# Performance work log

Measured on AMD Instinct MI355X. Metric: run time of the kernel, lower is better.

The kernel has to match this reference:

```python
import jax, jax.numpy as jnp
import numpy as np

WIN = 9  # local window size per spatial dim

def _boxfilter3d(x):
    k = jnp.ones((1, 1, WIN, WIN, WIN), x.dtype) / float(WIN ** 3)
    return jax.lax.conv_general_dilated(
        x, k, window_strides=(1, 1, 1), padding='SAME',
        dimension_numbers=('NCDHW', 'OIDHW', 'NCDHW'))

def setup_inputs() -> dict:
    key = jax.random.key(0)
    k1, k2 = jax.random.split(key)
    shape = (2, 1, 160, 192, 160)
    y_true = jax.random.uniform(k1, shape, dtype=jnp.float32)
    y_pred = jax.random.uniform(k2, shape, dtype=jnp.float32)
    return {"y_true": y_true, "y_pred": y_pred}

def reference(y_true, y_pred):
    Ii, Ji = y_true, y_pred
    mu1 = _boxfilter3d(Ii)
    mu2 = _boxfilter3d(Ji)
    sigma1_sq = _boxfilter3d(Ii * Ii) - mu1 * mu1
    sigma2_sq = _boxfilter3d(Ji * Ji) - mu2 * mu2
    sigma12 = _boxfilter3d(Ii * Ji) - mu1 * mu2
    cc = (sigma12 * sigma12) / (sigma1_sq * sigma2_sq + 1e-5)
    return -jnp.mean(cc)
```

## Files before the change

### kernel.cpp

```cpp
#include <hip/hip_runtime.h>

#define DD 160
#define HH 192
#define WW 160
#define HWs (HH * WW)
#define NTOT 9830400.0f
#define DOUT 10
#define NIT  18
#define NBLK 1920

#define SDRS 62
#define SDP  1492
#define HSRS 10
#define HSC  162
#define HSP  810

typedef float    v4 __attribute__((ext_vector_type(4)));
typedef _Float16 h4 __attribute__((ext_vector_type(4)));
typedef _Float16 h2 __attribute__((ext_vector_type(2)));
typedef _Float16 h8 __attribute__((ext_vector_type(8)));

__device__ __forceinline__ void block_sync_lds() {
    __builtin_amdgcn_s_waitcnt(0xc07f);
    __builtin_amdgcn_s_barrier();
}
__device__ __forceinline__ v4 up(h4 x) { return __builtin_convertvector(x, v4); }
__device__ __forceinline__ h4 dnp(v4 x) {
    h2 a = __builtin_bit_cast(h2, __builtin_amdgcn_cvt_pkrtz(x[0], x[1]));
    h2 b = __builtin_bit_cast(h2, __builtin_amdgcn_cvt_pkrtz(x[2], x[3]));
    return __builtin_shufflevector(a, b, 0, 1, 2, 3);
}

__global__ __launch_bounds__(256, 4) void kf(const float* __restrict__ I,
                                             const float* __restrict__ J,
                                             float* __restrict__ partial) {
    __shared__ __align__(16) h4 SDL[2 * SDP];
    __shared__ __align__(16) h4 HSL[2 * HSP];
    __shared__ float red[256];

    const int tid = threadIdx.x;
    const int bx = blockIdx.x, by = blockIdx.y, b = blockIdx.z;
    const int w0 = (bx % 5) * 32, h0 = (bx / 5) * 16;
    const int d0 = by * DOUT;
    const int bid = bx + 60 * (by + 16 * b);

    const int rt = tid ^ ((bx & 1) << 7);

    const bool p1 = rt < 240;
    const int r = rt / 10, g = rt % 10;
    const int gh = h0 - 4 + r, gw = w0 - 4 + g * 4;
    const bool colOK = p1 && gh >= 0 && gh < HH && gw >= 0 && gw < WW;
    const size_t colOff = (size_t)gh * WW + gw;
    const float* Ib = I + (size_t)b * DD * HWs + colOff;
    const float* Jb = J + (size_t)b * DD * HWs + colOff;
    const int sdwOff = r * SDRS + (r >> 3) * 2 + 6 * g;

    const bool p2 = rt < 100;
    const int g2 = rt % 10, ch2 = (rt / 10) % 5, hh0 = (rt / 50) * 8;
    const int sdrOff = hh0 * SDRS + (hh0 >> 3) * 2 + 6 * g2 +
                       (ch2 == 4 ? 4 + (g2 & 1) : ch2);
    const int hswOff = ch2 * HSC + hh0 * HSRS + g2;

    const bool p3 = rt >= 128;
    const int q3 = rt & 127;
    const int hh = q3 >> 3, sg = q3 & 7;
    const int hsrOff = hh * HSRS + sg;

    v4 sd0 = 0.f, sd1 = 0.f, sd2 = 0.f, sd3 = 0.f, sd4 = 0.f;
    h4 fI[9], fJ[9];
#pragma unroll
    for (int uu = 0; uu < 9; ++uu) { fI[uu] = (h4)(_Float16)0; fJ[uu] = (h4)(_Float16)0; }
    v4 pLI = 0.f, pLJ = 0.f;
    float acc = 0.f;
    const float inv = 1.0f / 729.0f;

    {
        const int si = d0 - 4;
        if (colOK && si >= 0) {
            pLI = *(const v4*)(Ib + (size_t)si * HWs);
            pLJ = *(const v4*)(Jb + (size_t)si * HWs);
        }
    }

    for (int tb = 0; tb < 27; tb += 9) {
#pragma unroll
        for (int u = 0; u < 9; ++u) {
            const int t = tb + u;
            if (t < NIT + 2) {
                if (t < NIT && p1) {
                    h4 cI = dnp(pLI), cJ = dnp(pLJ);
                    v4 aI = up(cI), aJ = up(cJ);
                    v4 dI = aI, dJv = aJ;
                    v4 dII = aI * aI, dJJ = aJ * aJ, dIJ = aI * aJ;
                    if (t >= 9) {
                        v4 bI = up(fI[u]), bJ = up(fJ[u]);
                        dI -= bI; dJv -= bJ;
                        dII -= bI * bI; dJJ -= bJ * bJ; dIJ -= bI * bJ;
                    }
                    fI[u] = cI; fJ[u] = cJ;
                    sd0 += dI; sd1 += dJv; sd2 += dII; sd3 += dJJ; sd4 += dIJ;
                    h4* const qb = &SDL[(t & 1) * SDP + sdwOff];
                    h4 c0 = dnp(sd0), c1 = dnp(sd1), c2 = dnp(sd2), c3 = dnp(sd3);
                    *(h8*)qb       = __builtin_shufflevector(c0, c1, 0,1,2,3,4,5,6,7);
                    *(h8*)(qb + 2) = __builtin_shufflevector(c2, c3, 0,1,2,3,4,5,6,7);
                    qb[4 + (g & 1)] = dnp(sd4);
                    pLI = 0.f; pLJ = 0.f;
                    const int sn = d0 - 3 + t;
                    if (t + 1 < NIT && colOK && sn >= 0 && sn < DD) {
                        pLI = *(const v4*)(Ib + (size_t)sn * HWs);
                        pLJ = *(const v4*)(Jb + (size_t)sn * HWs);
                    }
                }

                if (t >= 1 && t <= NIT && p2) {
                    const int par = (t - 1) & 1;
                    const h4* const sdr = &SDL[par * SDP + sdrOff];
                    h4* const hsw = &HSL[par * HSP + hswOff];
                    h4 s = sdr[0];
#pragma unroll
                    for (int k = 1; k < 9; ++k)
                        s += sdr[k * SDRS + (k >= 8 ? 2 : 0)];
                    hsw[0] = s;
#pragma unroll
                    for (int j = 1; j < 8; ++j) {
                        s += sdr[(j + 8) * SDRS + 2]
                           - sdr[(j - 1) * SDRS + (j - 1 >= 8 ? 2 : 0)];
                        hsw[j * HSRS] = s;
                    }
                }

                if (t >= 10 && p3) {
                    const h4* const hsr = &HSL[(t & 1) * HSP + hsrOff];
                    float w[5][4];
#pragma unroll
                    for (int c = 0; c < 5; ++c) {
                        v4 fa = up(hsr[c * HSC]);
                        v4 fb = up(hsr[c * HSC + 1]);
                        v4 fc = up(hsr[c * HSC + 2]);
                        float s = fa[0] + fa[1] + fa[2] + fa[3] +
                                  fb[0] + fb[1] + fb[2] + fb[3] + fc[0];
                        w[c][0] = s;
                        s += fc[1] - fa[0]; w[c][1] = s;
                        s += fc[2] - fa[1]; w[c][2] = s;
                        s += fc[3] - fa[2]; w[c][3] = s;
                    }
#pragma unroll
                    for (int e = 0; e < 4; ++e) {
                        float mu1 = w[0][e] * inv, mu2 = w[1][e] * inv;
                        float g1  = fmaf(-mu1, mu1, w[2][e] * inv);
                        float g2v = fmaf(-mu2, mu2, w[3][e] * inv);
                        float g12 = fmaf(-mu1, mu2, w[4][e] * inv);
                        acc += __fdividef(g12 * g12, fmaf(g1, g2v, 1e-5f));
                    }
                }

                block_sync_lds();
            }
        }
    }

    red[tid] = acc;
    __syncthreads();
    if (tid < 128) red[tid] += red[tid + 128];
    __syncthreads();
    if (tid < 64) {
        float a = red[tid] + red[tid + 64];
#pragma unroll
        for (int off = 32; off > 0; off >>= 1) a += __shfl_down(a, off);
        if (tid == 0) partial[bid] = a;
    }
}

__global__ void k3_final(const float* __restrict__ partial,
                         float* __restrict__ out) {
    __shared__ float r[1024];
    const int i = threadIdx.x;
    float v = (i < NBLK) ? partial[i] : 0.f;
    if (i + 1024 < NBLK) v += partial[i + 1024];
    r[i] = v;
    __syncthreads();
    for (int off = 512; off > 0; off >>= 1) {
        if (i < off) r[i] += r[i + off];
        __syncthreads();
    }
    if (i == 0) out[0] = -r[0] * (1.0f / NTOT);
}

extern "C" void kernel_launch(void* const* d_in, const int* in_sizes, int n_in,
                              void* d_out, int out_size, void* d_ws, size_t ws_size,
                              hipStream_t stream) {
    (void)in_sizes; (void)n_in; (void)out_size; (void)ws_size;
    const float* I = (const float*)d_in[0];
    const float* J = (const float*)d_in[1];
    float* out     = (float*)d_out;
    float* partial = (float*)d_ws;

    dim3 grid(60, 16, 2);
    kf<<<grid, 256, 0, stream>>>(I, J, partial);
    k3_final<<<1, 1024, 0, stream>>>(partial, out);
}
```

Measured before the change: 167.8 us.

## Reload outgoing depth slices from memory, store H-sums in fp32, remap blocks

Drops the register ring of fp16 input values for the sliding depth window and instead reloads the outgoing slice from global memory (likely served from cache). Input values are now used in fp32 without fp16 rounding. The horizontal partial sums go to LDS as fp32 rather than fp16, which doubles that buffer. Blocks move to a 1D grid with an XCD-aware interleaved tile mapping, and launch bounds drop to 3 waves per SIMD. The aim is to cut register pressure and improve L2 locality, at the cost of extra global loads and more LDS use.

```diff
diff --git a/kernel.cpp b/kernel.cpp
--- a/kernel.cpp
+++ b/kernel.cpp
@@ -31,18 +31,20 @@
     return __builtin_shufflevector(a, b, 0, 1, 2, 3);
 }
 
-__global__ __launch_bounds__(256, 4) void kf(const float* __restrict__ I,
+__global__ __launch_bounds__(256, 3) void kf(const float* __restrict__ I,
                                              const float* __restrict__ J,
                                              float* __restrict__ partial) {
     __shared__ __align__(16) h4 SDL[2 * SDP];
-    __shared__ __align__(16) h4 HSL[2 * HSP];
+    __shared__ __align__(16) v4 HSL[2 * HSP];
     __shared__ float red[256];
 
     const int tid = threadIdx.x;
-    const int bx = blockIdx.x, by = blockIdx.y, b = blockIdx.z;
+    const int wgid = blockIdx.x;
+    const int tl = (wgid & 7) * 240 + (wgid >> 3);
+    const int bx = tl % 60, by = (tl / 60) % 16, b = tl / 960;
     const int w0 = (bx % 5) * 32, h0 = (bx / 5) * 16;
     const int d0 = by * DOUT;
-    const int bid = bx + 60 * (by + 16 * b);
+    const int bid = tl;
 
     const int rt = tid ^ ((bx & 1) << 7);
 
@@ -67,10 +69,8 @@
     const int hsrOff = hh * HSRS + sg;
 
     v4 sd0 = 0.f, sd1 = 0.f, sd2 = 0.f, sd3 = 0.f, sd4 = 0.f;
-    h4 fI[9], fJ[9];
-#pragma unroll
-    for (int uu = 0; uu < 9; ++uu) { fI[uu] = (h4)(_Float16)0; fJ[uu] = (h4)(_Float16)0; }
     v4 pLI = 0.f, pLJ = 0.f;
+    v4 pOI = 0.f, pOJ = 0.f;
     float acc = 0.f;
     const float inv = 1.0f / 729.0f;
 
@@ -82,81 +82,78 @@
         }
     }
 
-    for (int tb = 0; tb < 27; tb += 9) {
 #pragma unroll
-        for (int u = 0; u < 9; ++u) {
-            const int t = tb + u;
-            if (t < NIT + 2) {
-                if (t < NIT && p1) {
-                    h4 cI = dnp(pLI), cJ = dnp(pLJ);
-                    v4 aI = up(cI), aJ = up(cJ);
-                    v4 dI = aI, dJv = aJ;
-                    v4 dII = aI * aI, dJJ = aJ * aJ, dIJ = aI * aJ;
-                    if (t >= 9) {
-                        v4 bI = up(fI[u]), bJ = up(fJ[u]);
-                        dI -= bI; dJv -= bJ;
-                        dII -= bI * bI; dJJ -= bJ * bJ; dIJ -= bI * bJ;
-                    }
-                    fI[u] = cI; fJ[u] = cJ;
-                    sd0 += dI; sd1 += dJv; sd2 += dII; sd3 += dJJ; sd4 += dIJ;
-                    h4* const qb = &SDL[(t & 1) * SDP + sdwOff];
-                    h4 c0 = dnp(sd0), c1 = dnp(sd1), c2 = dnp(sd2), c3 = dnp(sd3);
-                    *(h8*)qb       = __builtin_shufflevector(c0, c1, 0,1,2,3,4,5,6,7);
-                    *(h8*)(qb + 2) = __builtin_shufflevector(c2, c3, 0,1,2,3,4,5,6,7);
-                    qb[4 + (g & 1)] = dnp(sd4);
-                    pLI = 0.f; pLJ = 0.f;
-                    const int sn = d0 - 3 + t;
-                    if (t + 1 < NIT && colOK && sn >= 0 && sn < DD) {
-                        pLI = *(const v4*)(Ib + (size_t)sn * HWs);
-                        pLJ = *(const v4*)(Jb + (size_t)sn * HWs);
-                    }
-                }
-
-                if (t >= 1 && t <= NIT && p2) {
-                    const int par = (t - 1) & 1;
-                    const h4* const sdr = &SDL[par * SDP + sdrOff];
-                    h4* const hsw = &HSL[par * HSP + hswOff];
-                    h4 s = sdr[0];
-#pragma unroll
-                    for (int k = 1; k < 9; ++k)
-                        s += sdr[k * SDRS + (k >= 8 ? 2 : 0)];
-                    hsw[0] = s;
-#pragma unroll
-                    for (int j = 1; j < 8; ++j) {
-                        s += sdr[(j + 8) * SDRS + 2]
-                           - sdr[(j - 1) * SDRS + (j - 1 >= 8 ? 2 : 0)];
-                        hsw[j * HSRS] = s;
-                    }
-                }
-
-                if (t >= 10 && p3) {
-                    const h4* const hsr = &HSL[(t & 1) * HSP + hsrOff];
-                    float w[5][4];
-#pragma unroll
-                    for (int c = 0; c < 5; ++c) {
-                        v4 fa = up(hsr[c * HSC]);
-                        v4 fb = up(hsr[c * HSC + 1]);
-                        v4 fc = up(hsr[c * HSC + 2]);
-                        float s = fa[0] + fa[1] + fa[2] + fa[3] +
-                                  fb[0] + fb[1] + fb[2] + fb[3] + fc[0];
-                        w[c][0] = s;
-                        s += fc[1] - fa[0]; w[c][1] = s;
-                        s += fc[2] - fa[1]; w[c][2] = s;
-                        s += fc[3] - fa[2]; w[c][3] = s;
-                    }
-#pragma unroll
-                    for (int e = 0; e < 4; ++e) {
-                        float mu1 = w[0][e] * inv, mu2 = w[1][e] * inv;
-                        float g1  = fmaf(-mu1, mu1, w[2][e] * inv);
-                        float g2v = fmaf(-mu2, mu2, w[3][e] * inv);
-                        float g12 = fmaf(-mu1, mu2, w[4][e] * inv);
-                        acc += __fdividef(g12 * g12, fmaf(g1, g2v, 1e-5f));
-                    }
-                }
-
-                block_sync_lds();
+    for (int t = 0; t < NIT + 2; ++t) {
+        if (t < NIT && p1) {
+            const v4 cI = pLI, cJ = pLJ;
+            v4 dI = cI, dJv = cJ;
+            v4 dII = cI * cI, dJJ = cJ * cJ, dIJ = cI * cJ;
+            if (t >= 9) {
+                dI  -= pOI;        dJv -= pOJ;
+                dII -= pOI * pOI;  dJJ -= pOJ * pOJ;  dIJ -= pOI * pOJ;
+            }
+            sd0 += dI; sd1 += dJv; sd2 += dII; sd3 += dJJ; sd4 += dIJ;
+            h4* const qb = &SDL[(t & 1) * SDP + sdwOff];
+            h4 c0 = dnp(sd0), c1 = dnp(sd1), c2 = dnp(sd2), c3 = dnp(sd3);
+            *(h8*)qb       = __builtin_shufflevector(c0, c1, 0,1,2,3,4,5,6,7);
+            *(h8*)(qb + 2) = __builtin_shufflevector(c2, c3, 0,1,2,3,4,5,6,7);
+            qb[4 + (g & 1)] = dnp(sd4);
+            pLI = 0.f; pLJ = 0.f;
+            const int sn = d0 - 3 + t;
+            if (t + 1 < NIT && colOK && sn >= 0 && sn < DD) {
+                pLI = *(const v4*)(Ib + (size_t)sn * HWs);
+                pLJ = *(const v4*)(Jb + (size_t)sn * HWs);
+            }
+            pOI = 0.f; pOJ = 0.f;
+            const int so = d0 - 12 + t;
+            if (t >= 8 && t + 1 < NIT && colOK && so >= 0) {
+                pOI = *(const v4*)(Ib + (size_t)so * HWs);
+                pOJ = *(const v4*)(Jb + (size_t)so * HWs);
             }
         }
+
+        if (t >= 1 && t <= NIT && p2) {
+            const int par = (t - 1) & 1;
+            const h4* const sdr = &SDL[par * SDP + sdrOff];
+            v4* const hsw = &HSL[par * HSP + hswOff];
+            h4 s = sdr[0];
+#pragma unroll
+            for (int k = 1; k < 9; ++k)
+                s += sdr[k * SDRS + (k >= 8 ? 2 : 0)];
+            hsw[0] = up(s);
+#pragma unroll
+            for (int j = 1; j < 8; ++j) {
+                s += sdr[(j + 8) * SDRS + 2] - sdr[(j - 1) * SDRS];
+                hsw[j * HSRS] = up(s);
+            }
+        }
+
+        if (t >= 10 && p3) {
+            const v4* const hsr = &HSL[(t & 1) * HSP + hsrOff];
+            float w[5][4];
+#pragma unroll
+            for (int c = 0; c < 5; ++c) {
+                v4 fa = hsr[c * HSC];
+                v4 fb = hsr[c * HSC + 1];
+                v4 fc = hsr[c * HSC + 2];
+                float s = fa[0] + fa[1] + fa[2] + fa[3] +
+                          fb[0] + fb[1] + fb[2] + fb[3] + fc[0];
+                w[c][0] = s;
+                s += fc[1] - fa[0]; w[c][1] = s;
+                s += fc[2] - fa[1]; w[c][2] = s;
+                s += fc[3] - fa[2]; w[c][3] = s;
+            }
+#pragma unroll
+            for (int e = 0; e < 4; ++e) {
+                float mu1 = w[0][e] * inv, mu2 = w[1][e] * inv;
+                float g1  = fmaf(-mu1, mu1, w[2][e] * inv);
+                float g2v = fmaf(-mu2, mu2, w[3][e] * inv);
+                float g12 = fmaf(-mu1, mu2, w[4][e] * inv);
+                acc += __fdividef(g12 * g12, fmaf(g1, g2v, 1e-5f));
+            }
+        }
+
+        block_sync_lds();
     }
 
     red[tid] = acc;
@@ -195,7 +192,6 @@
     float* out     = (float*)d_out;
     float* partial = (float*)d_ws;
 
-    dim3 grid(60, 16, 2);
-    kf<<<grid, 256, 0, stream>>>(I, J, partial);
+    kf<<<dim3(NBLK), 256, 0, stream>>>(I, J, partial);
     k3_final<<<1, 1024, 0, stream>>>(partial, out);
 }
```

Result: faster. 150.7 us (-10.2%).
